# Kernel optimization log

Measured on AMD Instinct MI355X. Metric: run time of the kernel, lower is better.

## Reference

```python
import jax, jax.numpy as jnp
import numpy as np

C = 1024      # BIGNET_DIM
GROUPS = 256  # (1024*1024) / group_size(4096)

def _dequant(q4, norm):
    # q4: [GROUPS, 2048] ints in [0,256) packing two 4-bit codes per byte
    # (even positions = low nibble, odd positions = high nibble, as in
    #  block_quantize_4bit / block_dequantize_4bit). norm: [GROUPS, 1].
    lo = q4 % 16
    hi = q4 // 16
    q8 = jnp.stack([lo, hi], axis=-1).reshape(GROUPS, -1).astype(jnp.float32)  # [GROUPS, 4096]
    w = (q8 / 15.0 * 2.0 - 1.0) * norm
    return w.reshape(C, C)  # [out_features, in_features]

def setup_inputs() -> dict:
    key = jax.random.key(0)
    ks = jax.random.split(key, 6)
    x = jax.random.normal(ks[0], (16384, C), jnp.float32)
    wq4 = jax.random.randint(ks[1], (18, GROUPS, 2048), 0, 256, jnp.int32)
    wnorm = jax.random.uniform(ks[2], (18, GROUPS, 1), dtype=jnp.float32) * 0.05 + 1e-3
    lora_a = jax.random.normal(ks[3], (3, 32, C), jnp.float32) * 0.02
    lora_b = jax.random.normal(ks[4], (3, C, 32), jnp.float32) * 0.01
    ln_gamma = jnp.ones((5, C), jnp.float32)
    ln_beta = jnp.zeros((5, C), jnp.float32)
    return {"x": x, "wq4": wq4, "wnorm": wnorm, "lora_a": lora_a,
            "lora_b": lora_b, "ln_gamma": ln_gamma, "ln_beta": ln_beta}

def reference(x, wq4, wnorm, lora_a, lora_b, ln_gamma, ln_beta):
    def lin(h, i):
        # dequantize group-wise int4 weight, then linear (bias=False)
        return h @ _dequant(wq4[i], wnorm[i]).T

    def block(h, b, li):
        y = lin(h, 3 * b)
        if li is not None:  # QLoRALinear: parallel fp32 low-rank path
            y = y + (h @ lora_a[li].T) @ lora_b[li].T
        y = jax.nn.relu(y)
        y = jax.nn.relu(lin(y, 3 * b + 1))
        y = lin(y, 3 * b + 2)
        return y + h  # residual

    def ln(h, i):
        mu = jnp.mean(h, axis=-1, keepdims=True)
        var = jnp.mean((h - mu) ** 2, axis=-1, keepdims=True)
        return (h - mu) * jax.lax.rsqrt(var + 1e-5) * ln_gamma[i] + ln_beta[i]

    h = block(x, 0, 0); h = ln(h, 0)
    h = block(h, 1, None); h = ln(h, 1)
    h = block(h, 2, 1); h = ln(h, 2)
    h = block(h, 3, None); h = ln(h, 3)
    h = block(h, 4, 2); h = ln(h, 4)
    h = block(h, 5, None)
    return h
```

## Files before the change

kernel.cpp:

```cpp
#include <hip/hip_runtime.h>

typedef __bf16 bf16x8 __attribute__((ext_vector_type(8)));
typedef float f32x4 __attribute__((ext_vector_type(4)));

__device__ __forceinline__ unsigned short f32_to_bf16u(float f) {
  unsigned int u = __float_as_uint(f);
  u += 0x7fffu + ((u >> 16) & 1u);
  return (unsigned short)(u >> 16);
}
__device__ __forceinline__ float bf16u_to_f32(unsigned short s) {
  return __uint_as_float((unsigned int)s << 16);
}

__device__ __forceinline__ void async_copy16(const void* gptr, void* lptr) {
  __builtin_amdgcn_global_load_lds(
      (__attribute__((address_space(1))) void*)(unsigned long long)gptr,
      (__attribute__((address_space(3))) void*)(unsigned long long)lptr,
      16, 0, 0);
}

__global__ __launch_bounds__(256) void lora_ba_kernel(
    const float* __restrict__ lora_a, const float* __restrict__ lora_b,
    float* __restrict__ Wba)
{
  const int bid = blockIdx.x;
  const int li = bid >> 10;
  const int o = bid & 1023;
  const float* B = lora_b + li * 32768 + o * 32;
  const float* A = lora_a + li * 32768;
  const int c = threadIdx.x * 4;
  float4 acc = {0.f, 0.f, 0.f, 0.f};
#pragma unroll
  for (int r = 0; r < 32; r++) {
    const float br = B[r];
    const float4 a = *(const float4*)&A[r * 1024 + c];
    acc.x += br * a.x; acc.y += br * a.y; acc.z += br * a.z; acc.w += br * a.w;
  }
  *(float4*)&Wba[((size_t)li << 20) + o * 1024 + c] = acc;
}

__global__ __launch_bounds__(256) void dequant_kernel(
    const int* __restrict__ wq4, const float* __restrict__ wnorm,
    const float* __restrict__ Wba, unsigned short* __restrict__ Wd)
{
  const int gi = blockIdx.x * 256 + threadIdx.x;
  const int w = gi >> 19;
  const int rem = gi & 524287;
  const int q = wq4[gi];
  const float norm = wnorm[(w << 8) + (rem >> 11)];
  float w0 = ((float)(q & 15) * (2.0f / 15.0f) - 1.0f) * norm;
  float w1 = ((float)(q >> 4) * (2.0f / 15.0f) - 1.0f) * norm;
  const int p = rem << 1;
  const int li = (w == 0) ? 0 : (w == 6) ? 1 : (w == 12) ? 2 : -1;
  if (li >= 0) {
    const float2 ba = *(const float2*)&Wba[((size_t)li << 20) + p];
    w0 += ba.x;
    w1 += ba.y;
  }
  const unsigned int packed =
      ((unsigned int)f32_to_bf16u(w1) << 16) | (unsigned int)f32_to_bf16u(w0);
  *(unsigned int*)&Wd[((size_t)w << 20) + p] = packed;
}

__global__ __launch_bounds__(256) void cast_bf16_kernel(
    const float* __restrict__ x, unsigned short* __restrict__ o)
{
  const int i = blockIdx.x * 256 + threadIdx.x;
  const float4 v = ((const float4*)x)[i];
  ushort4 b;
  b.x = f32_to_bf16u(v.x);
  b.y = f32_to_bf16u(v.y);
  b.z = f32_to_bf16u(v.z);
  b.w = f32_to_bf16u(v.w);
  ((ushort4*)o)[i] = b;
}

template <int EPIL>
__global__ __launch_bounds__(256, 4) void gemm_bt(
    const unsigned short* __restrict__ A, const unsigned short* __restrict__ W,
    void* __restrict__ Out, const unsigned short* __restrict__ Res)
{
  constexpr int K = 1024;
  constexpr int N = 1024;
  __shared__ unsigned short As[128 * 64];
  __shared__ unsigned short Ws[128 * 64];

  const int tid = threadIdx.x;
  const int lane = tid & 63;
  const int wave = tid >> 6;

  const int bid = blockIdx.x;
  const int xcd = bid & 7;
  const int j = bid >> 3;
  const int m0 = (xcd * 16 + (j >> 3)) * 128;
  const int n0 = (j & 7) * 128;

  const int wm = (wave >> 1) * 64;
  const int wn = (wave & 1) * 64;

  f32x4 acc[4][4];
#pragma unroll
  for (int i = 0; i < 4; i++)
#pragma unroll
    for (int jj = 0; jj < 4; jj++) acc[i][jj] = (f32x4){0.f, 0.f, 0.f, 0.f};

  const int arow = tid >> 3;
  const int acol8 = (tid & 7) ^ (arow & 7);
  const unsigned short* Ag = A + (size_t)(m0 + arow) * K + acol8 * 8;
  const unsigned short* Wg = W + (size_t)(n0 + arow) * K + acol8 * 8;
  unsigned short* Asd = &As[tid * 8];
  unsigned short* Wsd = &Ws[tid * 8];

  const int fr = lane & 15;
  const int q = lane >> 4;

  for (int k0 = 0; k0 < K; k0 += 64) {
#pragma unroll
    for (int i = 0; i < 4; i++)
      async_copy16(Ag + (size_t)i * 32 * K + k0, Asd + i * 2048);
#pragma unroll
    for (int i = 0; i < 4; i++)
      async_copy16(Wg + (size_t)i * 32 * K + k0, Wsd + i * 2048);
    __syncthreads();
#pragma unroll
    for (int h = 0; h < 2; h++) {
      const int kk8 = q + h * 4;
      bf16x8 a[4], b[4];
#pragma unroll
      for (int i = 0; i < 4; i++) {
        const int row = wm + i * 16 + fr;
        a[i] = *(const bf16x8*)&As[row * 64 + ((kk8 ^ (fr & 7)) << 3)];
      }
#pragma unroll
      for (int jj = 0; jj < 4; jj++) {
        const int row = wn + jj * 16 + fr;
        b[jj] = *(const bf16x8*)&Ws[row * 64 + ((kk8 ^ (fr & 7)) << 3)];
      }
#pragma unroll
      for (int i = 0; i < 4; i++)
#pragma unroll
        for (int jj = 0; jj < 4; jj++)
          acc[i][jj] = __builtin_amdgcn_mfma_f32_16x16x32_bf16(a[i], b[jj], acc[i][jj], 0, 0, 0);
    }
    __syncthreads();
  }

  const int rq = q * 4;
#pragma unroll
  for (int i = 0; i < 4; i++) {
#pragma unroll
    for (int r = 0; r < 4; r++) {
      const int m = m0 + wm + i * 16 + rq + r;
#pragma unroll
      for (int jj = 0; jj < 4; jj++) {
        const int n = n0 + wn + jj * 16 + fr;
        float v = acc[i][jj][r];
        if (EPIL == 0) {
          v = v > 0.f ? v : 0.f;
          ((unsigned short*)Out)[(size_t)m * N + n] = f32_to_bf16u(v);
        } else if (EPIL == 1) {
          v += bf16u_to_f32(Res[(size_t)m * N + n]);
          ((unsigned short*)Out)[(size_t)m * N + n] = f32_to_bf16u(v);
        } else {
          v += bf16u_to_f32(Res[(size_t)m * N + n]);
          ((float*)Out)[(size_t)m * N + n] = v;
        }
      }
    }
  }
}

__global__ __launch_bounds__(256) void ln_kernel(
    const unsigned short* __restrict__ s_bf, const float* __restrict__ gamma,
    const float* __restrict__ beta, unsigned short* __restrict__ h_bf)
{
  const int row = blockIdx.x;
  const int tid = threadIdx.x;
  const size_t base = (size_t)row * 1024;
  const ushort4 u = ((const ushort4*)(s_bf + base))[tid];
  float v0 = bf16u_to_f32(u.x), v1 = bf16u_to_f32(u.y);
  float v2 = bf16u_to_f32(u.z), v3 = bf16u_to_f32(u.w);
  float s = v0 + v1 + v2 + v3;
  float s2 = v0 * v0 + v1 * v1 + v2 * v2 + v3 * v3;
#pragma unroll
  for (int off = 32; off > 0; off >>= 1) {
    s += __shfl_down(s, off, 64);
    s2 += __shfl_down(s2, off, 64);
  }
  __shared__ float red[8];
  if ((tid & 63) == 0) {
    red[tid >> 6] = s;
    red[4 + (tid >> 6)] = s2;
  }
  __syncthreads();
  s = red[0] + red[1] + red[2] + red[3];
  s2 = red[4] + red[5] + red[6] + red[7];
  const float mu = s * (1.0f / 1024.0f);
  const float var = s2 * (1.0f / 1024.0f) - mu * mu;
  const float rs = rsqrtf(var + 1e-5f);
  const float4 g = ((const float4*)gamma)[tid];
  const float4 bb = ((const float4*)beta)[tid];
  ushort4 ob;
  ob.x = f32_to_bf16u((v0 - mu) * rs * g.x + bb.x);
  ob.y = f32_to_bf16u((v1 - mu) * rs * g.y + bb.y);
  ob.z = f32_to_bf16u((v2 - mu) * rs * g.z + bb.z);
  ob.w = f32_to_bf16u((v3 - mu) * rs * g.w + bb.w);
  ((ushort4*)(h_bf + base))[tid] = ob;
}

extern "C" void kernel_launch(void* const* d_in, const int* in_sizes, int n_in,
                              void* d_out, int out_size, void* d_ws, size_t ws_size,
                              hipStream_t stream)
{
  const float* x = (const float*)d_in[0];
  const int* wq4 = (const int*)d_in[1];
  const float* wnorm = (const float*)d_in[2];
  const float* lora_a = (const float*)d_in[3];
  const float* lora_b = (const float*)d_in[4];
  const float* ln_g = (const float*)d_in[5];
  const float* ln_b = (const float*)d_in[6];
  float* out = (float*)d_out;

  char* ws = (char*)d_ws;
  unsigned short* Wd   = (unsigned short*)(ws);
  unsigned short* x_bf = (unsigned short*)(ws + 37748736);
  unsigned short* t1   = (unsigned short*)(ws + 71303168);
  unsigned short* t2   = (unsigned short*)(ws + 104857600);
  unsigned short* s_bf = (unsigned short*)(ws + 138412032);
  unsigned short* h_bf = (unsigned short*)(ws + 171966464);
  float* Wba           = (float*)(ws + 138412032);

  lora_ba_kernel<<<3072, 256, 0, stream>>>(lora_a, lora_b, Wba);
  dequant_kernel<<<36864, 256, 0, stream>>>(wq4, wnorm, Wba, Wd);
  cast_bf16_kernel<<<16384, 256, 0, stream>>>(x, x_bf);

  const unsigned short* hb = x_bf;
  const unsigned short* hres = x_bf;
  for (int b = 0; b < 6; b++) {
    const unsigned short* W0 = Wd + (size_t)(3 * b + 0) * 1048576;
    const unsigned short* W1 = Wd + (size_t)(3 * b + 1) * 1048576;
    const unsigned short* W2 = Wd + (size_t)(3 * b + 2) * 1048576;
    gemm_bt<0><<<1024, 256, 0, stream>>>(hb, W0, t1, nullptr);
    gemm_bt<0><<<1024, 256, 0, stream>>>(t1, W1, t2, nullptr);
    if (b < 5) {
      gemm_bt<1><<<1024, 256, 0, stream>>>(t2, W2, s_bf, hres);
      ln_kernel<<<16384, 256, 0, stream>>>(s_bf, ln_g + b * 1024, ln_b + b * 1024, h_bf);
      hb = h_bf;
      hres = h_bf;
    } else {
      gemm_bt<2><<<1024, 256, 0, stream>>>(t2, W2, out, hres);
    }
  }
  (void)in_sizes; (void)n_in; (void)out_size; (void)ws_size;
}
```

Baseline: 909.8 us.

## Rewrite GEMM as 256x256 tile, 8-wave, double-buffered LDS pipeline

Replaces the 128x128, 4-wave, single-buffered GEMM with a 256x256 tile computed by 8 waves, each holding a 128x64 accumulator. The LDS is double-buffered into A and B halves, and async global-to-LDS copies for the next k-slices are interleaved with MFMA phases using explicit barriers, waitcnt and setprio. This targets the exposed load latency and the low arithmetic intensity of the old kernel. In exchange, register pressure is much higher, LDS use is 128KB per block, and the grid drops to 256 blocks, which means only one wave of blocks across the CUs.

```diff
diff --git a/kernel.cpp b/kernel.cpp
--- a/kernel.cpp
+++ b/kernel.cpp
@@ -76,85 +76,161 @@
 }
 
 template <int EPIL>
-__global__ __launch_bounds__(256, 4) void gemm_bt(
+__global__ __launch_bounds__(512, 2) void gemm_bt(
     const unsigned short* __restrict__ A, const unsigned short* __restrict__ W,
     void* __restrict__ Out, const unsigned short* __restrict__ Res)
 {
   constexpr int K = 1024;
   constexpr int N = 1024;
-  __shared__ unsigned short As[128 * 64];
-  __shared__ unsigned short Ws[128 * 64];
+  __shared__ unsigned short lds[2][4][8192];
 
   const int tid = threadIdx.x;
   const int lane = tid & 63;
-  const int wave = tid >> 6;
+  const int wv = tid >> 6;
+  const int wm = wv >> 2;
+  const int wn = wv & 3;
 
   const int bid = blockIdx.x;
-  const int xcd = bid & 7;
-  const int j = bid >> 3;
-  const int m0 = (xcd * 16 + (j >> 3)) * 128;
-  const int n0 = (j & 7) * 128;
-
-  const int wm = (wave >> 1) * 64;
-  const int wn = (wave & 1) * 64;
-
-  f32x4 acc[4][4];
-#pragma unroll
-  for (int i = 0; i < 4; i++)
-#pragma unroll
-    for (int jj = 0; jj < 4; jj++) acc[i][jj] = (f32x4){0.f, 0.f, 0.f, 0.f};
-
-  const int arow = tid >> 3;
-  const int acol8 = (tid & 7) ^ (arow & 7);
-  const unsigned short* Ag = A + (size_t)(m0 + arow) * K + acol8 * 8;
-  const unsigned short* Wg = W + (size_t)(n0 + arow) * K + acol8 * 8;
-  unsigned short* Asd = &As[tid * 8];
-  unsigned short* Wsd = &Ws[tid * 8];
+  const int l = (bid & 7) * 32 + (bid >> 3);
+  const int m0 = (l >> 2) << 8;
+  const int n0 = (l & 3) << 8;
 
   const int fr = lane & 15;
   const int q = lane >> 4;
-
-  for (int k0 = 0; k0 < K; k0 += 64) {
-#pragma unroll
-    for (int i = 0; i < 4; i++)
-      async_copy16(Ag + (size_t)i * 32 * K + k0, Asd + i * 2048);
-#pragma unroll
-    for (int i = 0; i < 4; i++)
-      async_copy16(Wg + (size_t)i * 32 * K + k0, Wsd + i * 2048);
-    __syncthreads();
-#pragma unroll
-    for (int h = 0; h < 2; h++) {
-      const int kk8 = q + h * 4;
-      bf16x8 a[4], b[4];
-#pragma unroll
-      for (int i = 0; i < 4; i++) {
-        const int row = wm + i * 16 + fr;
-        a[i] = *(const bf16x8*)&As[row * 64 + ((kk8 ^ (fr & 7)) << 3)];
-      }
-#pragma unroll
-      for (int jj = 0; jj < 4; jj++) {
-        const int row = wn + jj * 16 + fr;
-        b[jj] = *(const bf16x8*)&Ws[row * 64 + ((kk8 ^ (fr & 7)) << 3)];
-      }
-#pragma unroll
-      for (int i = 0; i < 4; i++)
-#pragma unroll
-        for (int jj = 0; jj < 4; jj++)
-          acc[i][jj] = __builtin_amdgcn_mfma_f32_16x16x32_bf16(a[i], b[jj], acc[i][jj], 0, 0, 0);
-    }
-    __syncthreads();
-  }
-
-  const int rq = q * 4;
-#pragma unroll
-  for (int i = 0; i < 4; i++) {
-#pragma unroll
-    for (int r = 0; r < 4; r++) {
-      const int m = m0 + wm + i * 16 + rq + r;
-#pragma unroll
-      for (int jj = 0; jj < 4; jj++) {
-        const int n = n0 + wn + jj * 16 + fr;
-        float v = acc[i][jj][r];
+  const int fr7 = fr & 7;
+
+  const int srow = tid >> 3;
+  const int schk = (tid & 7) ^ (srow & 7);
+  const unsigned short* Asrc = A + (size_t)(m0 + srow) * K + schk * 8;
+  const int nb0 = ((srow >> 5) << 6) + (srow & 31);
+  const unsigned short* Wsrc = W + (size_t)(n0 + nb0) * K + schk * 8;
+
+#define STAGE_A(mq, dbuf, kt)                                          \
+  do {                                                                 \
+    const unsigned short* s_ = Asrc + (size_t)(mq) * 64 * K + (kt);    \
+    unsigned short* d_ = &lds[dbuf][(mq) ? 2 : 0][tid * 8];            \
+    async_copy16(s_, d_);                                              \
+    async_copy16(s_ + (size_t)128 * K, d_ + 4096);                     \
+  } while (0)
+#define STAGE_B(nq, dbuf, kt)                                          \
+  do {                                                                 \
+    const unsigned short* s_ = Wsrc + (size_t)(nq) * 32 * K + (kt);    \
+    unsigned short* d_ = &lds[dbuf][(nq) ? 3 : 1][tid * 8];            \
+    async_copy16(s_, d_);                                              \
+    async_copy16(s_ + (size_t)128 * K, d_ + 4096);                     \
+  } while (0)
+
+  const int a_lane = (wm * 64 + fr) * 64;
+  const int b_lane = (wn * 32 + fr) * 64;
+  const int c0 = (q ^ fr7) << 3;
+  const int c1 = ((4 + q) ^ fr7) << 3;
+
+#define LDA4(dbuf, mq)                                                               \
+  do {                                                                               \
+    _Pragma("unroll") for (int ri = 0; ri < 4; ++ri) {                               \
+      af[ri][0] = *(const bf16x8*)&lds[dbuf][(mq) ? 2 : 0][a_lane + ri * 1024 + c0]; \
+      af[ri][1] = *(const bf16x8*)&lds[dbuf][(mq) ? 2 : 0][a_lane + ri * 1024 + c1]; \
+    }                                                                                \
+  } while (0)
+#define LDB2(dst, dbuf, nq)                                                          \
+  do {                                                                               \
+    _Pragma("unroll") for (int rj = 0; rj < 2; ++rj) {                               \
+      dst[rj][0] = *(const bf16x8*)&lds[dbuf][(nq) ? 3 : 1][b_lane + rj * 1024 + c0];\
+      dst[rj][1] = *(const bf16x8*)&lds[dbuf][(nq) ? 3 : 1][b_lane + rj * 1024 + c1];\
+    }                                                                                \
+  } while (0)
+
+#define MFMA16(ib, jb, BB)                                                    \
+  do {                                                                        \
+    _Pragma("unroll") for (int i2 = 0; i2 < 4; ++i2)                          \
+    _Pragma("unroll") for (int j2 = 0; j2 < 2; ++j2) {                        \
+      acc[(ib) + i2][(jb) + j2] = __builtin_amdgcn_mfma_f32_16x16x32_bf16(    \
+          af[i2][0], BB[j2][0], acc[(ib) + i2][(jb) + j2], 0, 0, 0);          \
+      acc[(ib) + i2][(jb) + j2] = __builtin_amdgcn_mfma_f32_16x16x32_bf16(    \
+          af[i2][1], BB[j2][1], acc[(ib) + i2][(jb) + j2], 0, 0, 0);          \
+    }                                                                         \
+  } while (0)
+
+#define PHASE_MFMA(ib, jb, BB)                           \
+  do {                                                   \
+    __builtin_amdgcn_s_barrier();                        \
+    asm volatile("s_waitcnt lgkmcnt(0)" ::: "memory");   \
+    __builtin_amdgcn_s_setprio(1);                       \
+    MFMA16(ib, jb, BB);                                  \
+    __builtin_amdgcn_s_setprio(0);                       \
+    __builtin_amdgcn_s_barrier();                        \
+  } while (0)
+#define PHASE_MFMA_VM(ib, jb, BB)                        \
+  do {                                                   \
+    __builtin_amdgcn_s_barrier();                        \
+    asm volatile("s_waitcnt lgkmcnt(0)" ::: "memory");   \
+    __builtin_amdgcn_s_setprio(1);                       \
+    MFMA16(ib, jb, BB);                                  \
+    __builtin_amdgcn_s_setprio(0);                       \
+    asm volatile("s_waitcnt vmcnt(6)" ::: "memory");     \
+    __builtin_amdgcn_s_barrier();                        \
+  } while (0)
+
+  f32x4 acc[8][4];
+#pragma unroll
+  for (int a_ = 0; a_ < 8; ++a_)
+#pragma unroll
+    for (int b_ = 0; b_ < 4; ++b_) acc[a_][b_] = (f32x4){0.f, 0.f, 0.f, 0.f};
+
+  bf16x8 af[4][2], bf0[2][2], bf1[2][2];
+
+  STAGE_A(0, 0, 0);
+  STAGE_B(0, 0, 0);
+  STAGE_A(1, 0, 0);
+  STAGE_B(1, 0, 0);
+  STAGE_A(0, 1, 64);
+  STAGE_B(0, 1, 64);
+  STAGE_A(1, 1, 64);
+  asm volatile("s_waitcnt vmcnt(6)" ::: "memory");
+  __builtin_amdgcn_s_barrier();
+
+  for (int it = 0; it < K / 128; ++it) {
+    const int kb = it * 128;
+    const int k2 = (kb + 128 < K) ? (kb + 128) : (K - 64);
+    const int k3 = (kb + 192 < K) ? (kb + 192) : (K - 64);
+
+    LDA4(0, 0);
+    LDB2(bf0, 0, 0);
+    STAGE_B(1, 1, kb + 64);
+    PHASE_MFMA(0, 0, bf0);
+    LDB2(bf1, 0, 1);
+    STAGE_A(0, 0, k2);
+    PHASE_MFMA(0, 2, bf1);
+    LDA4(0, 1);
+    STAGE_B(0, 0, k2);
+    PHASE_MFMA(4, 0, bf0);
+    STAGE_A(1, 0, k2);
+    PHASE_MFMA_VM(4, 2, bf1);
+    LDA4(1, 0);
+    LDB2(bf0, 1, 0);
+    STAGE_B(1, 0, k2);
+    PHASE_MFMA(0, 0, bf0);
+    LDB2(bf1, 1, 1);
+    STAGE_A(0, 1, k3);
+    PHASE_MFMA(0, 2, bf1);
+    LDA4(1, 1);
+    STAGE_B(0, 1, k3);
+    PHASE_MFMA(4, 0, bf0);
+    STAGE_A(1, 1, k3);
+    PHASE_MFMA_VM(4, 2, bf1);
+  }
+
+  const int mb = m0 + wm * 128 + q * 4;
+  const int nb = n0 + wn * 64 + fr;
+#pragma unroll
+  for (int i2 = 0; i2 < 8; ++i2) {
+#pragma unroll
+    for (int r = 0; r < 4; ++r) {
+      const int m = mb + i2 * 16 + r;
+#pragma unroll
+      for (int j2 = 0; j2 < 4; ++j2) {
+        const int n = nb + j2 * 16;
+        float v = acc[i2][j2][r];
         if (EPIL == 0) {
           v = v > 0.f ? v : 0.f;
           ((unsigned short*)Out)[(size_t)m * N + n] = f32_to_bf16u(v);
@@ -168,6 +244,13 @@
       }
     }
   }
+#undef STAGE_A
+#undef STAGE_B
+#undef LDA4
+#undef LDB2
+#undef MFMA16
+#undef PHASE_MFMA
+#undef PHASE_MFMA_VM
 }
 
 __global__ __launch_bounds__(256) void ln_kernel(
@@ -240,15 +323,15 @@
     const unsigned short* W0 = Wd + (size_t)(3 * b + 0) * 1048576;
     const unsigned short* W1 = Wd + (size_t)(3 * b + 1) * 1048576;
     const unsigned short* W2 = Wd + (size_t)(3 * b + 2) * 1048576;
-    gemm_bt<0><<<1024, 256, 0, stream>>>(hb, W0, t1, nullptr);
-    gemm_bt<0><<<1024, 256, 0, stream>>>(t1, W1, t2, nullptr);
+    gemm_bt<0><<<256, 512, 0, stream>>>(hb, W0, t1, nullptr);
+    gemm_bt<0><<<256, 512, 0, stream>>>(t1, W1, t2, nullptr);
     if (b < 5) {
-      gemm_bt<1><<<1024, 256, 0, stream>>>(t2, W2, s_bf, hres);
+      gemm_bt<1><<<256, 512, 0, stream>>>(t2, W2, s_bf, hres);
       ln_kernel<<<16384, 256, 0, stream>>>(s_bf, ln_g + b * 1024, ln_b + b * 1024, h_bf);
       hb = h_bf;
       hres = h_bf;
     } else {
-      gemm_bt<2><<<1024, 256, 0, stream>>>(t2, W2, out, hres);
+      gemm_bt<2><<<256, 512, 0, stream>>>(t2, W2, out, hres);
     }
   }
   (void)in_sizes; (void)n_in; (void)out_size; (void)ws_size;
```

After: 875.1 us. -3.8%, faster.

## Rewrite GEMM as 256x128 tile, 8-wave, double-buffered pipelined kernel

Applied to the files above, without the earlier changes.

Replaces the 128x128 single-buffer GEMM with a 512-thread block computing a 128x256 output tile. Global-to-LDS async copies for the next K-slices are interleaved with MFMA sub-phases across two LDS buffers, and s_setprio is raised around the MFMAs. The aim is to hide load latency behind compute and cut the redundant A/W reads. The price is more LDS per block, lower occupancy, and heavy barrier use whose correctness depends on fragile vmcnt accounting.

```diff
diff --git a/kernel.cpp b/kernel.cpp
--- a/kernel.cpp
+++ b/kernel.cpp
@@ -76,85 +76,152 @@
 }
 
 template <int EPIL>
-__global__ __launch_bounds__(256, 4) void gemm_bt(
+__global__ __launch_bounds__(512, 2) void gemm_bt(
     const unsigned short* __restrict__ A, const unsigned short* __restrict__ W,
     void* __restrict__ Out, const unsigned short* __restrict__ Res)
 {
   constexpr int K = 1024;
   constexpr int N = 1024;
-  __shared__ unsigned short As[128 * 64];
-  __shared__ unsigned short Ws[128 * 64];
+  __shared__ unsigned short lds[2][3][8192];
 
   const int tid = threadIdx.x;
   const int lane = tid & 63;
-  const int wave = tid >> 6;
+  const int wv = tid >> 6;
+  const int wm = wv >> 2;
+  const int wn = wv & 3;
 
   const int bid = blockIdx.x;
-  const int xcd = bid & 7;
-  const int j = bid >> 3;
-  const int m0 = (xcd * 16 + (j >> 3)) * 128;
-  const int n0 = (j & 7) * 128;
-
-  const int wm = (wave >> 1) * 64;
-  const int wn = (wave & 1) * 64;
-
-  f32x4 acc[4][4];
-#pragma unroll
-  for (int i = 0; i < 4; i++)
-#pragma unroll
-    for (int jj = 0; jj < 4; jj++) acc[i][jj] = (f32x4){0.f, 0.f, 0.f, 0.f};
-
-  const int arow = tid >> 3;
-  const int acol8 = (tid & 7) ^ (arow & 7);
-  const unsigned short* Ag = A + (size_t)(m0 + arow) * K + acol8 * 8;
-  const unsigned short* Wg = W + (size_t)(n0 + arow) * K + acol8 * 8;
-  unsigned short* Asd = &As[tid * 8];
-  unsigned short* Wsd = &Ws[tid * 8];
+  const int l = (bid & 7) * 64 + (bid >> 3);
+  const int m0 = (l >> 2) << 7;
+  const int n0 = (l & 3) << 8;
 
   const int fr = lane & 15;
   const int q = lane >> 4;
-
-  for (int k0 = 0; k0 < K; k0 += 64) {
-#pragma unroll
-    for (int i = 0; i < 4; i++)
-      async_copy16(Ag + (size_t)i * 32 * K + k0, Asd + i * 2048);
-#pragma unroll
-    for (int i = 0; i < 4; i++)
-      async_copy16(Wg + (size_t)i * 32 * K + k0, Wsd + i * 2048);
-    __syncthreads();
-#pragma unroll
-    for (int h = 0; h < 2; h++) {
-      const int kk8 = q + h * 4;
-      bf16x8 a[4], b[4];
-#pragma unroll
-      for (int i = 0; i < 4; i++) {
-        const int row = wm + i * 16 + fr;
-        a[i] = *(const bf16x8*)&As[row * 64 + ((kk8 ^ (fr & 7)) << 3)];
-      }
-#pragma unroll
-      for (int jj = 0; jj < 4; jj++) {
-        const int row = wn + jj * 16 + fr;
-        b[jj] = *(const bf16x8*)&Ws[row * 64 + ((kk8 ^ (fr & 7)) << 3)];
-      }
-#pragma unroll
-      for (int i = 0; i < 4; i++)
-#pragma unroll
-        for (int jj = 0; jj < 4; jj++)
-          acc[i][jj] = __builtin_amdgcn_mfma_f32_16x16x32_bf16(a[i], b[jj], acc[i][jj], 0, 0, 0);
-    }
-    __syncthreads();
-  }
-
-  const int rq = q * 4;
-#pragma unroll
-  for (int i = 0; i < 4; i++) {
-#pragma unroll
-    for (int r = 0; r < 4; r++) {
-      const int m = m0 + wm + i * 16 + rq + r;
-#pragma unroll
-      for (int jj = 0; jj < 4; jj++) {
-        const int n = n0 + wn + jj * 16 + fr;
-        float v = acc[i][jj][r];
+  const int fr7 = fr & 7;
+
+  const int srow = tid >> 3;
+  const int schk = (tid & 7) ^ (srow & 7);
+  const unsigned short* Asrc = A + (size_t)(m0 + srow) * K + schk * 8;
+  const unsigned short* Wsrc = W + (size_t)(n0 + srow) * K + schk * 8;
+
+#define STAGE_A(dbuf, kt)                                              \
+  do {                                                                 \
+    const unsigned short* s_ = Asrc + (kt);                            \
+    unsigned short* d_ = &lds[dbuf][0][tid * 8];                       \
+    async_copy16(s_, d_);                                              \
+    async_copy16(s_ + (size_t)64 * K, d_ + 4096);                      \
+  } while (0)
+#define STAGE_B0(dbuf, kt)                                             \
+  do {                                                                 \
+    const unsigned short* s_ = Wsrc + (kt);                            \
+    unsigned short* d_ = &lds[dbuf][1][tid * 8];                       \
+    async_copy16(s_, d_);                                              \
+    async_copy16(s_ + (size_t)64 * K, d_ + 4096);                      \
+  } while (0)
+#define STAGE_B1(dbuf, kt)                                             \
+  do {                                                                 \
+    const unsigned short* s_ = Wsrc + (size_t)128 * K + (kt);          \
+    unsigned short* d_ = &lds[dbuf][2][tid * 8];                       \
+    async_copy16(s_, d_);                                              \
+    async_copy16(s_ + (size_t)64 * K, d_ + 4096);                      \
+  } while (0)
+
+  const int c0 = (q ^ fr7) << 3;
+  const int c1 = ((4 + q) ^ fr7) << 3;
+  const int breg = 1 + (wn >> 1);
+  const int a_base = (wm * 64 + fr) * 64;
+  const int b_base = ((wn & 1) * 64 + fr) * 64;
+
+#define LDA(dbuf, mq)                                                  \
+  do {                                                                 \
+    _Pragma("unroll") for (int i2 = 0; i2 < 2; ++i2) {                 \
+      const int ro = a_base + ((mq) * 32 + i2 * 16) * 64;              \
+      af[i2][0] = *(const bf16x8*)&lds[dbuf][0][ro + c0];              \
+      af[i2][1] = *(const bf16x8*)&lds[dbuf][0][ro + c1];              \
+    }                                                                  \
+  } while (0)
+#define LDB(dst, dbuf, nq)                                             \
+  do {                                                                 \
+    _Pragma("unroll") for (int j2 = 0; j2 < 2; ++j2) {                 \
+      const int ro = b_base + ((nq) * 32 + j2 * 16) * 64;              \
+      dst[j2][0] = *(const bf16x8*)&lds[dbuf][breg][ro + c0];          \
+      dst[j2][1] = *(const bf16x8*)&lds[dbuf][breg][ro + c1];          \
+    }                                                                  \
+  } while (0)
+
+#define MFMA8(mq, nq, BB)                                                     \
+  do {                                                                        \
+    __builtin_amdgcn_s_setprio(1);                                            \
+    _Pragma("unroll") for (int i2 = 0; i2 < 2; ++i2)                          \
+    _Pragma("unroll") for (int j2 = 0; j2 < 2; ++j2) {                        \
+      acc[(mq)*2 + i2][(nq)*2 + j2] = __builtin_amdgcn_mfma_f32_16x16x32_bf16(\
+          af[i2][0], BB[j2][0], acc[(mq)*2 + i2][(nq)*2 + j2], 0, 0, 0);      \
+      acc[(mq)*2 + i2][(nq)*2 + j2] = __builtin_amdgcn_mfma_f32_16x16x32_bf16(\
+          af[i2][1], BB[j2][1], acc[(mq)*2 + i2][(nq)*2 + j2], 0, 0, 0);      \
+    }                                                                         \
+    __builtin_amdgcn_s_setprio(0);                                            \
+  } while (0)
+
+#define BAR __builtin_amdgcn_s_barrier()
+#define LG0 asm volatile("s_waitcnt lgkmcnt(0)" ::: "memory")
+#define VM4 asm volatile("s_waitcnt vmcnt(4)" ::: "memory")
+
+  f32x4 acc[4][4];
+#pragma unroll
+  for (int a_ = 0; a_ < 4; ++a_)
+#pragma unroll
+    for (int b_ = 0; b_ < 4; ++b_) acc[a_][b_] = (f32x4){0.f, 0.f, 0.f, 0.f};
+
+  bf16x8 af[2][2], bfA[2][2], bfB[2][2];
+
+  STAGE_A(0, 0);
+  STAGE_B0(0, 0);
+  STAGE_B1(0, 0);
+  STAGE_A(1, 64);
+  STAGE_B0(1, 64);
+  asm volatile("s_waitcnt vmcnt(4)" ::: "memory");
+  BAR;
+
+  for (int it = 0; it < K / 128; ++it) {
+    const int kb = it * 128;
+    const int k2 = (kb + 128 < K) ? (kb + 128) : (K - 64);
+    const int k3 = (kb + 192 < K) ? (kb + 192) : (K - 64);
+
+    LDA(0, 0);
+    LDB(bfA, 0, 0);
+    STAGE_B1(1, kb + 64);
+    BAR; LG0; MFMA8(0, 0, bfA); BAR;
+    LDB(bfB, 0, 1);
+    BAR; LG0; MFMA8(0, 1, bfB); BAR;
+    LDA(0, 1);
+    STAGE_B0(0, k2);
+    BAR; LG0; MFMA8(1, 0, bfA); BAR;
+    STAGE_A(0, k2);
+    BAR; LG0; MFMA8(1, 1, bfB); VM4; BAR;
+    LDA(1, 0);
+    LDB(bfA, 1, 0);
+    STAGE_B1(0, k2);
+    BAR; LG0; MFMA8(0, 0, bfA); BAR;
+    LDB(bfB, 1, 1);
+    BAR; LG0; MFMA8(0, 1, bfB); BAR;
+    LDA(1, 1);
+    STAGE_B0(1, k3);
+    BAR; LG0; MFMA8(1, 0, bfA); BAR;
+    STAGE_A(1, k3);
+    BAR; LG0; MFMA8(1, 1, bfB); VM4; BAR;
+  }
+
+  const int mb = m0 + wm * 64 + q * 4;
+  const int nb = n0 + wn * 64 + fr;
+#pragma unroll
+  for (int i2 = 0; i2 < 4; ++i2) {
+#pragma unroll
+    for (int r = 0; r < 4; ++r) {
+      const int m = mb + i2 * 16 + r;
+#pragma unroll
+      for (int j2 = 0; j2 < 4; ++j2) {
+        const int n = nb + j2 * 16;
+        float v = acc[i2][j2][r];
         if (EPIL == 0) {
           v = v > 0.f ? v : 0.f;
           ((unsigned short*)Out)[(size_t)m * N + n] = f32_to_bf16u(v);
@@ -168,6 +235,15 @@
       }
     }
   }
+#undef STAGE_A
+#undef STAGE_B0
+#undef STAGE_B1
+#undef LDA
+#undef LDB
+#undef MFMA8
+#undef BAR
+#undef LG0
+#undef VM4
 }
 
 __global__ __launch_bounds__(256) void ln_kernel(
@@ -240,15 +316,15 @@
     const unsigned short* W0 = Wd + (size_t)(3 * b + 0) * 1048576;
     const unsigned short* W1 = Wd + (size_t)(3 * b + 1) * 1048576;
     const unsigned short* W2 = Wd + (size_t)(3 * b + 2) * 1048576;
-    gemm_bt<0><<<1024, 256, 0, stream>>>(hb, W0, t1, nullptr);
-    gemm_bt<0><<<1024, 256, 0, stream>>>(t1, W1, t2, nullptr);
+    gemm_bt<0><<<512, 512, 0, stream>>>(hb, W0, t1, nullptr);
+    gemm_bt<0><<<512, 512, 0, stream>>>(t1, W1, t2, nullptr);
     if (b < 5) {
-      gemm_bt<1><<<1024, 256, 0, stream>>>(t2, W2, s_bf, hres);
+      gemm_bt<1><<<512, 512, 0, stream>>>(t2, W2, s_bf, hres);
       ln_kernel<<<16384, 256, 0, stream>>>(s_bf, ln_g + b * 1024, ln_b + b * 1024, h_bf);
       hb = h_bf;
       hres = h_bf;
     } else {
-      gemm_bt<2><<<1024, 256, 0, stream>>>(t2, W2, out, hres);
+      gemm_bt<2><<<512, 512, 0, stream>>>(t2, W2, out, hres);
     }
   }
   (void)in_sizes; (void)n_in; (void)out_size; (void)ws_size;
```

Measured after the change: 980.5 us. 7.8% more time.
